# Optimization experiments

Hardware: AMD Instinct MI355X
Metric: run time of the kernel (lower is better)

The kernel has to match this reference:

```python
import jax, jax.numpy as jnp
import numpy as np

N_QUBITS = 4
N_LAYERS = 3
H_IMG = 512

# ---------- 4-qubit statevector simulator, batched over P patches ----------

def _apply_1q(psi, U, w):
    # shared 2x2 gate U on wire w; psi: (P,2,2,2,2)
    psi = jnp.moveaxis(psi, 1 + w, -1)
    psi = jnp.einsum('ij,...j->...i', U, psi)
    return jnp.moveaxis(psi, -1, 1 + w)

def _apply_1q_batched(psi, U, w):
    # per-patch gate U: (P,2,2)
    psi = jnp.moveaxis(psi, 1 + w, -1)
    psi = jnp.einsum('pij,p...j->p...i', U, psi)
    return jnp.moveaxis(psi, -1, 1 + w)

def _apply_cnot(psi, c, t):
    psi = jnp.moveaxis(psi, (1 + c, 1 + t), (-2, -1))
    top = psi[..., 0:1, :]
    bot = psi[..., 1:2, ::-1]  # X on target when control=1
    psi = jnp.concatenate([top, bot], axis=-2)
    return jnp.moveaxis(psi, (-2, -1), (1 + c, 1 + t))

def _rx(theta):
    # AngleEmbedding default rotation='X'; theta: (P,) -> (P,2,2)
    h = theta * 0.5
    c = jnp.cos(h).astype(jnp.complex64)
    s = (-1j * jnp.sin(h)).astype(jnp.complex64)
    return jnp.stack([jnp.stack([c, s], -1), jnp.stack([s, c], -1)], -2)

def _rot(phi, theta, omega):
    # PennyLane Rot = RZ(omega) RY(theta) RZ(phi)
    c = jnp.cos(theta * 0.5)
    s = jnp.sin(theta * 0.5)
    em = jnp.exp(-0.5j * (phi + omega))
    ep = jnp.exp(0.5j * (phi + omega))
    fm = jnp.exp(0.5j * (phi - omega))
    fp = jnp.exp(-0.5j * (phi - omega))
    row0 = jnp.stack([em * c, -fm * s])
    row1 = jnp.stack([fp * s, ep * c])
    return jnp.stack([row0, row1]).astype(jnp.complex64)

def _qsim(inputs, weights):
    # inputs: (P,4) angles; weights: (3,4,3) Rot params -> (P,4) PauliZ expvals
    P = inputs.shape[0]
    psi = jnp.zeros((P, 2, 2, 2, 2), jnp.complex64).at[:, 0, 0, 0, 0].set(1.0)
    for w in range(N_QUBITS):
        psi = _apply_1q_batched(psi, _rx(inputs[:, w]), w)
    for l in range(N_LAYERS):
        for w in range(N_QUBITS):
            psi = _apply_1q(psi, _rot(weights[l, w, 0], weights[l, w, 1], weights[l, w, 2]), w)
        r = (l % (N_QUBITS - 1)) + 1  # StronglyEntanglingLayers default ranges
        for w in range(N_QUBITS):
            psi = _apply_cnot(psi, w, (w + r) % N_QUBITS)
    probs = psi.real ** 2 + psi.imag ** 2  # (P,2,2,2,2)
    ez = []
    for w in range(N_QUBITS):
        axes = tuple(a for a in range(1, 5) if a != 1 + w)
        p = probs.sum(axes)  # (P,2)
        ez.append(p[:, 0] - p[:, 1])
    return jnp.stack(ez, -1)  # (P,4)

def _qconv(x, q_weights):
    img = x[0, 0]  # (H,W)
    a = img[:-1, :-1]; b = img[:-1, 1:]; c = img[1:, :-1]; d = img[1:, 1:]
    Hm, Wm = a.shape
    patches = jnp.stack([a, b, c, d], -1).reshape(-1, 4)  # row-major 2x2 flatten
    ez = _qsim(patches, q_weights)  # (P,4)
    return ez.reshape(Hm, Wm, 4).transpose(2, 0, 1)[None]  # (1,4,Hm,Wm)

# ---------- classical layers ----------

def _conv(x, w, b):
    y = jax.lax.conv_general_dilated(x, w, (1, 1), 'VALID',
                                     dimension_numbers=('NCHW', 'OIHW', 'NCHW'))
    return y + b[None, :, None, None]

def _maxpool2(x):
    return jax.lax.reduce_window(x, -jnp.inf, jax.lax.max,
                                 (1, 1, 2, 2), (1, 1, 2, 2), 'VALID')

def _adaptive_max(x, out):
    H, W = x.shape[-2], x.shape[-1]
    rows = []
    for i in range(out):
        si, ei = (i * H) // out, -(-((i + 1) * H) // out)
        cols = []
        for j in range(out):
            sj, ej = (j * W) // out, -(-((j + 1) * W) // out)
            cols.append(x[..., si:ei, sj:ej].max((-2, -1)))
        rows.append(jnp.stack(cols, -1))
    return jnp.stack(rows, -2)


def setup_inputs() -> dict:
    key = jax.random.key(0)
    ks = jax.random.split(key, 10)
    x = jax.random.normal(ks[0], (1, 1, H_IMG, H_IMG), jnp.float32)
    q_weights = jax.random.uniform(ks[1], (N_LAYERS, N_QUBITS, 3), jnp.float32,
                                   0.0, 2.0 * np.pi)
    conv2_w = jax.random.normal(ks[2], (20, 4, 5, 5), jnp.float32) * 0.05
    conv2_b = jax.random.normal(ks[3], (20,), jnp.float32) * 0.05
    conv3_w = jax.random.normal(ks[4], (40, 20, 3, 3), jnp.float32) * 0.05
    conv3_b = jax.random.normal(ks[5], (40,), jnp.float32) * 0.05
    fc1_w = jax.random.normal(ks[6], (64, 640), jnp.float32) * 0.05
    fc1_b = jax.random.normal(ks[7], (64,), jnp.float32) * 0.05
    fc2_w = jax.random.normal(ks[8], (10, 64), jnp.float32) * 0.05
    fc2_b = jax.random.normal(ks[9], (10,), jnp.float32) * 0.05
    return {'x': x, 'q_weights': q_weights,
            'conv2_w': conv2_w, 'conv2_b': conv2_b,
            'conv3_w': conv3_w, 'conv3_b': conv3_b,
            'fc1_w': fc1_w, 'fc1_b': fc1_b,
            'fc2_w': fc2_w, 'fc2_b': fc2_b}


def reference(x, q_weights, conv2_w, conv2_b, conv3_w, conv3_b,
              fc1_w, fc1_b, fc2_w, fc2_b):
    h = _maxpool2(jax.nn.sigmoid(_qconv(x, q_weights)))        # (1,4,255,255)
    h = _maxpool2(jax.nn.relu(_conv(h, conv2_w, conv2_b)))      # (1,20,125,125)
    h = _adaptive_max(jax.nn.relu(_conv(h, conv3_w, conv3_b)), 4)  # (1,40,4,4)
    h = h.reshape(-1, 640)
    h = jax.nn.relu(h @ fc1_w.T + fc1_b)
    return h @ fc2_w.T + fc2_b  # (1,10)
```

## Files before the change

kernel.cpp:

```cpp
#include <hip/hip_runtime.h>
#include <math.h>

#define IMG 512
#define QO  255
#define QP  256
#define C2H 125
#define C2S 128
#define C3H 123

template<int M_>
__device__ inline void rot_regs(float2* a, float2 U00, float2 U01, float2 U10, float2 U11) {
    #pragma unroll
    for (int s = 0; s < 16; ++s) {
        if (!(s & M_)) {
            float2 a0 = a[s], a1 = a[s | M_];
            a[s]      = make_float2(U00.x*a0.x - U00.y*a0.y + U01.x*a1.x - U01.y*a1.y,
                                    U00.x*a0.y + U00.y*a0.x + U01.x*a1.y + U01.y*a1.x);
            a[s | M_] = make_float2(U10.x*a0.x - U10.y*a0.y + U11.x*a1.x - U11.y*a1.y,
                                    U10.x*a0.y + U10.y*a0.x + U11.x*a1.y + U11.y*a1.x);
        }
    }
}
template<int MC, int MT>
__device__ inline void cnot_regs(float2* a) {
    #pragma unroll
    for (int s = 0; s < 16; ++s) {
        if ((s & MC) && !(s & MT)) {
            float2 t = a[s]; a[s] = a[s | MT]; a[s | MT] = t;
        }
    }
}
__device__ inline void rot_gate_params(float phi, float th, float om,
                                       float2& U00, float2& U01, float2& U10, float2& U11) {
    float ch, sh, ca, sa, cb, sb;
    __sincosf(0.5f * th, &sh, &ch);
    __sincosf(0.5f * (phi + om), &sa, &ca);
    __sincosf(0.5f * (phi - om), &sb, &cb);
    U00 = make_float2( ca*ch, -sa*ch);
    U01 = make_float2(-cb*sh, -sb*sh);
    U10 = make_float2( cb*sh, -sb*sh);
    U11 = make_float2( ca*ch,  sa*ch);
}

__device__ __constant__ int UP1[10] = {0,0,0,0,1,1,1,2,2,3};
__device__ __constant__ int UP2[10] = {0,1,2,3,1,2,3,2,3,3};

__global__ __launch_bounds__(256) void qconv_pool(const float* __restrict__ img,
                                                  const float* __restrict__ qw,
                                                  float* __restrict__ out) {
    __shared__ float2 Ms[256];
    __shared__ float4 G4[100];
    int tid = threadIdx.x;

    if (tid < 16) {
        float2 a[16];
        #pragma unroll
        for (int s = 0; s < 16; ++s) a[s] = make_float2(s == tid ? 1.f : 0.f, 0.f);
        float2 U00, U01, U10, U11;
#define ROTG(L, W) rot_gate_params(qw[((L)*4+(W))*3+0], qw[((L)*4+(W))*3+1], qw[((L)*4+(W))*3+2], U00,U01,U10,U11); \
                   rot_regs<(1 << (3-(W)))>(a, U00, U01, U10, U11);
        ROTG(0,0) ROTG(0,1) ROTG(0,2) ROTG(0,3)
        cnot_regs<8,4>(a); cnot_regs<4,2>(a); cnot_regs<2,1>(a); cnot_regs<1,8>(a);
        ROTG(1,0) ROTG(1,1) ROTG(1,2) ROTG(1,3)
        cnot_regs<8,2>(a); cnot_regs<4,1>(a); cnot_regs<2,8>(a); cnot_regs<1,4>(a);
        ROTG(2,0) ROTG(2,1) ROTG(2,2) ROTG(2,3)
        cnot_regs<8,1>(a); cnot_regs<4,8>(a); cnot_regs<2,4>(a); cnot_regs<1,2>(a);
#undef ROTG
        int pc4 = __popc(tid) & 3;
        #pragma unroll
        for (int row = 0; row < 16; ++row) {
            float2 v = a[row], o;
            if      (pc4 == 0) o = v;
            else if (pc4 == 1) o = make_float2( v.y, -v.x);
            else if (pc4 == 2) o = make_float2(-v.x, -v.y);
            else               o = make_float2(-v.y,  v.x);
            Ms[row * 16 + tid] = o;
        }
    }
    __syncthreads();

    if (tid < 100) {
        int al = tid / 10, be = tid - 10 * (tid / 10);
        int u = UP1[al], up = UP2[al], v = UP1[be], vp = UP2[be];
        float s0 = 0.f, s1 = 0.f, s2 = 0.f, s3 = 0.f;
        for (int ci = 0; ci < 2; ++ci) {
            if (ci == 1 && u == up) break;
            int a1 = ci ? up : u, a2 = ci ? u : up;
            for (int cj = 0; cj < 2; ++cj) {
                if (cj == 1 && v == vp) break;
                int b1 = cj ? vp : v, b2 = cj ? v : vp;
                int k = a1 * 4 + b1, kp = a2 * 4 + b2;
                #pragma unroll
                for (int r = 0; r < 16; ++r) {
                    float2 m1 = Ms[r * 16 + k], m2 = Ms[r * 16 + kp];
                    float p = m1.x * m2.x + m1.y * m2.y;
                    s0 += (r & 8) ? -p : p;
                    s1 += (r & 4) ? -p : p;
                    s2 += (r & 2) ? -p : p;
                    s3 += (r & 1) ? -p : p;
                }
            }
        }
        G4[tid] = make_float4(s0, s1, s2, s3);
    }
    __syncthreads();

    int gid = blockIdx.x * 256 + tid;
    if (gid >= QO * QO) return;
    int i = gid / QO, j = gid - i * QO;
    int r0 = 2 * i, c0 = 2 * j;

    float cs[3][3], sn[3][3];
    #pragma unroll
    for (int rr = 0; rr < 3; ++rr)
        #pragma unroll
        for (int cc = 0; cc < 3; ++cc) {
            float v = img[(r0 + rr) * IMG + c0 + cc];
            __sincosf(0.5f * v, &sn[rr][cc], &cs[rr][cc]);
        }

    float tv[3][2][4];
    #pragma unroll
    for (int rr = 0; rr < 3; ++rr)
        #pragma unroll
        for (int pc = 0; pc < 2; ++pc) {
            tv[rr][pc][0] = cs[rr][pc] * cs[rr][pc+1];
            tv[rr][pc][1] = cs[rr][pc] * sn[rr][pc+1];
            tv[rr][pc][2] = sn[rr][pc] * cs[rr][pc+1];
            tv[rr][pc][3] = sn[rr][pc] * sn[rr][pc+1];
        }

    float mx0 = -1e30f, mx1 = -1e30f, mx2 = -1e30f, mx3 = -1e30f;

    #pragma unroll
    for (int pr = 0; pr < 2; ++pr) {
        #pragma unroll
        for (int pc = 0; pc < 2; ++pc) {
            float q23[10];
            #pragma unroll
            for (int be = 0; be < 10; ++be)
                q23[be] = tv[pr+1][pc][UP1[be]] * tv[pr+1][pc][UP2[be]];

            float e0 = 0.f, e1 = 0.f, e2 = 0.f, e3 = 0.f;
            #pragma unroll
            for (int al = 0; al < 10; ++al) {
                float pa = tv[pr][pc][UP1[al]] * tv[pr][pc][UP2[al]];
                #pragma unroll
                for (int be = 0; be < 10; ++be) {
                    float4 g = G4[al * 10 + be];
                    float pq = pa * q23[be];
                    e0 = fmaf(g.x, pq, e0);
                    e1 = fmaf(g.y, pq, e1);
                    e2 = fmaf(g.z, pq, e2);
                    e3 = fmaf(g.w, pq, e3);
                }
            }
            mx0 = fmaxf(mx0, e0);
            mx1 = fmaxf(mx1, e1);
            mx2 = fmaxf(mx2, e2);
            mx3 = fmaxf(mx3, e3);
        }
    }

    int o = i * QP + j;
    out[0 * QP * QP + o] = 1.f / (1.f + __expf(-mx0));
    out[1 * QP * QP + o] = 1.f / (1.f + __expf(-mx1));
    out[2 * QP * QP + o] = 1.f / (1.f + __expf(-mx2));
    out[3 * QP * QP + o] = 1.f / (1.f + __expf(-mx3));
}

__global__ __launch_bounds__(256) void conv2_pool(const float* __restrict__ in,
                                                  const float* __restrict__ w,
                                                  const float* __restrict__ b,
                                                  float* __restrict__ out,
                                                  float* __restrict__ am) {
    __shared__ float W[100];
    __shared__ float Bv;
    int oc = blockIdx.y;
    if (threadIdx.x < 100) W[threadIdx.x] = w[oc * 100 + threadIdx.x];
    if (threadIdx.x == 0) Bv = b[oc];
    if (blockIdx.x == 0 && oc == 0) {
        for (int e = threadIdx.x; e < 640; e += 256) am[e] = 0.f;
    }
    __syncthreads();

    int sp = blockIdx.x * 256 + threadIdx.x;
    if (sp >= C2H * C2H) return;
    int i = sp / C2H, j = sp - i * C2H;

    float a00 = 0.f, a01 = 0.f, a10 = 0.f, a11 = 0.f;
    #pragma unroll
    for (int ic = 0; ic < 4; ++ic) {
        const float* ip = in + ic * QP * QP + (2 * i) * QP + 2 * j;
        float win[6][6];
        #pragma unroll
        for (int y = 0; y < 6; ++y) {
            #pragma unroll
            for (int h = 0; h < 3; ++h) {
                float2 v = *(const float2*)(ip + y * QP + 2 * h);
                win[y][2*h]   = v.x;
                win[y][2*h+1] = v.y;
            }
        }
        #pragma unroll
        for (int ky = 0; ky < 5; ++ky) {
            #pragma unroll
            for (int kx = 0; kx < 5; ++kx) {
                float wv = W[ic * 25 + ky * 5 + kx];
                a00 = fmaf(win[ky][kx],     wv, a00);
                a01 = fmaf(win[ky][kx+1],   wv, a01);
                a10 = fmaf(win[ky+1][kx],   wv, a10);
                a11 = fmaf(win[ky+1][kx+1], wv, a11);
            }
        }
    }
    float m = fmaxf(fmaxf(a00, a01), fmaxf(a10, a11));
    out[oc * C2H * C2S + i * C2S + j] = fmaxf(m + Bv, 0.f);
}

__global__ __launch_bounds__(256) void conv3_amax(const float* __restrict__ in,
                                                  const float* __restrict__ w,
                                                  const float* __restrict__ b,
                                                  int* __restrict__ am) {
    __shared__ float4 W4[180];
    __shared__ int bm[64];
    int og = blockIdx.y, oc0 = og * 4;
    if (threadIdx.x < 180) {
        int rr = threadIdx.x;
        const float* wb = w + oc0 * 180 + rr;
        W4[rr] = make_float4(wb[0], wb[180], wb[360], wb[540]);
    }
    if (threadIdx.x < 64) bm[threadIdx.x] = 0;
    __syncthreads();

    int sp = blockIdx.x * 256 + threadIdx.x;
    if (sp < C3H * C3H) {
        int y = sp / C3H, x = sp - y * C3H;

        float acc0 = 0.f, acc1 = 0.f, acc2 = 0.f, acc3 = 0.f;
        #pragma unroll
        for (int ic = 0; ic < 20; ++ic) {
            const float* ip = in + ic * C2H * C2S + y * C2S + x;
            float v[3][3];
            #pragma unroll
            for (int ky = 0; ky < 3; ++ky)
                #pragma unroll
                for (int kx = 0; kx < 3; ++kx)
                    v[ky][kx] = ip[ky * C2S + kx];
            #pragma unroll
            for (int kk = 0; kk < 9; ++kk) {
                float4 wv = W4[ic * 9 + kk];
                float iv = v[kk / 3][kk % 3];
                acc0 = fmaf(iv, wv.x, acc0);
                acc1 = fmaf(iv, wv.y, acc1);
                acc2 = fmaf(iv, wv.z, acc2);
                acc3 = fmaf(iv, wv.w, acc3);
            }
        }
        acc0 = fmaxf(acc0 + b[oc0 + 0], 0.f);
        acc1 = fmaxf(acc1 + b[oc0 + 1], 0.f);
        acc2 = fmaxf(acc2 + b[oc0 + 2], 0.f);
        acc3 = fmaxf(acc3 + b[oc0 + 3], 0.f);

        const int bs[4] = {0, 30, 61, 92};
        const int be[4] = {31, 62, 93, 123};
        #pragma unroll
        for (int yb = 0; yb < 4; ++yb) {
            if (y >= bs[yb] && y < be[yb]) {
                #pragma unroll
                for (int xb = 0; xb < 4; ++xb) {
                    if (x >= bs[xb] && x < be[xb]) {
                        int bin = yb * 4 + xb;
                        atomicMax(&bm[0 * 16 + bin], __float_as_int(acc0));
                        atomicMax(&bm[1 * 16 + bin], __float_as_int(acc1));
                        atomicMax(&bm[2 * 16 + bin], __float_as_int(acc2));
                        atomicMax(&bm[3 * 16 + bin], __float_as_int(acc3));
                    }
                }
            }
        }
    }
    __syncthreads();
    if (threadIdx.x < 64) {
        int v = bm[threadIdx.x];
        if (v != 0)
            atomicMax(&am[(oc0 + (threadIdx.x >> 4)) * 16 + (threadIdx.x & 15)], v);
    }
}

__global__ void fc_k(const float* __restrict__ h, const float* __restrict__ w1,
                     const float* __restrict__ b1, const float* __restrict__ w2,
                     const float* __restrict__ b2, float* __restrict__ out) {
    __shared__ float hh[640];
    __shared__ float h1[64];
    int t = threadIdx.x;
    for (int e = t; e < 640; e += 256) hh[e] = h[e];
    __syncthreads();

    int r = t >> 2, q = t & 3;
    const float4* wr = (const float4*)(w1 + r * 640 + q * 160);
    const float*  hp = hh + q * 160;
    float acc = 0.f;
    #pragma unroll 4
    for (int n = 0; n < 40; ++n) {
        float4 wv = wr[n];
        acc = fmaf(wv.x, hp[n*4+0], acc);
        acc = fmaf(wv.y, hp[n*4+1], acc);
        acc = fmaf(wv.z, hp[n*4+2], acc);
        acc = fmaf(wv.w, hp[n*4+3], acc);
    }
    acc += __shfl_xor(acc, 1, 64);
    acc += __shfl_xor(acc, 2, 64);
    if (q == 0) h1[r] = fmaxf(acc + b1[r], 0.f);
    __syncthreads();

    if (t < 10) {
        float o = b2[t];
        #pragma unroll 8
        for (int n = 0; n < 64; ++n) o = fmaf(h1[n], w2[t * 64 + n], o);
        out[t] = o;
    }
}

extern "C" void kernel_launch(void* const* d_in, const int* in_sizes, int n_in,
                              void* d_out, int out_size, void* d_ws, size_t ws_size,
                              hipStream_t stream) {
    const float* x   = (const float*)d_in[0];
    const float* qw  = (const float*)d_in[1];
    const float* c2w = (const float*)d_in[2];
    const float* c2b = (const float*)d_in[3];
    const float* c3w = (const float*)d_in[4];
    const float* c3b = (const float*)d_in[5];
    const float* f1w = (const float*)d_in[6];
    const float* f1b = (const float*)d_in[7];
    const float* f2w = (const float*)d_in[8];
    const float* f2b = (const float*)d_in[9];
    float* out = (float*)d_out;

    float* wsf   = (float*)d_ws;
    float* qout  = wsf;
    float* c2out = qout + 4 * QP * QP;
    float* am    = c2out + 20 * C2H * C2S;

    qconv_pool<<<(QO * QO + 255) / 256, 256, 0, stream>>>(x, qw, qout);
    conv2_pool<<<dim3((C2H * C2H + 255) / 256, 20), 256, 0, stream>>>(qout, c2w, c2b, c2out, am);
    conv3_amax<<<dim3((C3H * C3H + 255) / 256, 10), 256, 0, stream>>>(c2out, c3w, c3b, (int*)am);
    fc_k<<<1, 256, 0, stream>>>(am, f1w, f1b, f2w, f2b, out);
}
```

Baseline: 134.5 us.

## Fuse all four stages into one persistent kernel with grid barriers

Replaces the four kernel launches with a single persistent kernel of 256 blocks. Software grid barriers built on global atomics separate the qconv, conv2, conv3 and FC stages. Shared memory is overlaid through a union, and conv2 and conv3 work is distributed with grid-stride loops. The aim is to remove launch overhead and inter-kernel gaps. In exchange it adds a memset plus barrier spin costs and relies on all 256 blocks being co-resident. qconv needs 255 blocks' worth of work, so one block idles at the barrier, and the fixed 256-block grid limits parallelism in the conv stages.

```diff
diff --git a/kernel.cpp b/kernel.cpp
--- a/kernel.cpp
+++ b/kernel.cpp
@@ -7,6 +7,8 @@
 #define C2H 125
 #define C2S 128
 #define C3H 123
+#define NB  256
+#define NT  256
 
 template<int M_>
 __device__ inline void rot_regs(float2* a, float2 U00, float2 U01, float2 U10, float2 U11) {
@@ -45,11 +47,41 @@
 __device__ __constant__ int UP1[10] = {0,0,0,0,1,1,1,2,2,3};
 __device__ __constant__ int UP2[10] = {0,1,2,3,1,2,3,2,3,3};
 
-__global__ __launch_bounds__(256) void qconv_pool(const float* __restrict__ img,
-                                                  const float* __restrict__ qw,
-                                                  float* __restrict__ out) {
-    __shared__ float2 Ms[256];
-    __shared__ float4 G4[100];
+__device__ __forceinline__ void grid_barrier(int* bar) {
+    __syncthreads();
+    if (threadIdx.x == 0) {
+        __threadfence();
+        if (atomicAdd(bar, 1) == NB - 1) {
+            atomicAdd(bar, NB);
+        } else {
+            while (__hip_atomic_load(bar, __ATOMIC_RELAXED,
+                                     __HIP_MEMORY_SCOPE_AGENT) < 2 * NB)
+                __builtin_amdgcn_s_sleep(8);
+        }
+        __threadfence();
+    }
+    __syncthreads();
+}
+
+union SmemU {
+    struct { float2 Ms[256]; float4 G4[100]; } A;
+    struct { float  W[2000]; float  B[20];  } Bs;
+    struct { float4 W4[180]; int    bm[64]; } C;
+    struct { float  hh[640]; float  h1[64]; } D;
+};
+
+__global__ __launch_bounds__(NT) void fused_net(
+        const float* __restrict__ img, const float* __restrict__ qw,
+        const float* __restrict__ c2w, const float* __restrict__ c2b,
+        const float* __restrict__ c3w, const float* __restrict__ c3b,
+        const float* __restrict__ f1w, const float* __restrict__ f1b,
+        const float* __restrict__ f2w, const float* __restrict__ f2b,
+        float* __restrict__ ws, float* __restrict__ out) {
+    __shared__ SmemU sm;
+    int* bar    = (int*)ws;
+    float* am   = ws + 16;
+    float* qout = ws + 16 + 640;
+    float* c2o  = qout + 4 * QP * QP;
     int tid = threadIdx.x;
 
     if (tid < 16) {
@@ -74,11 +106,10 @@
             else if (pc4 == 1) o = make_float2( v.y, -v.x);
             else if (pc4 == 2) o = make_float2(-v.x, -v.y);
             else               o = make_float2(-v.y,  v.x);
-            Ms[row * 16 + tid] = o;
-        }
-    }
-    __syncthreads();
-
+            sm.A.Ms[row * 16 + tid] = o;
+        }
+    }
+    __syncthreads();
     if (tid < 100) {
         int al = tid / 10, be = tid - 10 * (tid / 10);
         int u = UP1[al], up = UP2[al], v = UP1[be], vp = UP2[be];
@@ -92,7 +123,7 @@
                 int k = a1 * 4 + b1, kp = a2 * 4 + b2;
                 #pragma unroll
                 for (int r = 0; r < 16; ++r) {
-                    float2 m1 = Ms[r * 16 + k], m2 = Ms[r * 16 + kp];
+                    float2 m1 = sm.A.Ms[r * 16 + k], m2 = sm.A.Ms[r * 16 + kp];
                     float p = m1.x * m2.x + m1.y * m2.y;
                     s0 += (r & 8) ? -p : p;
                     s1 += (r & 4) ? -p : p;
@@ -101,224 +132,197 @@
                 }
             }
         }
-        G4[tid] = make_float4(s0, s1, s2, s3);
-    }
-    __syncthreads();
-
-    int gid = blockIdx.x * 256 + tid;
-    if (gid >= QO * QO) return;
-    int i = gid / QO, j = gid - i * QO;
-    int r0 = 2 * i, c0 = 2 * j;
-
-    float cs[3][3], sn[3][3];
-    #pragma unroll
-    for (int rr = 0; rr < 3; ++rr)
+        sm.A.G4[tid] = make_float4(s0, s1, s2, s3);
+    }
+    __syncthreads();
+
+    {
+        int gid = blockIdx.x * NT + tid;
+        if (gid < QO * QO) {
+            int i = gid / QO, j = gid - i * QO;
+            int r0 = 2 * i, c0 = 2 * j;
+            float cs[3][3], sn[3][3];
+            #pragma unroll
+            for (int rr = 0; rr < 3; ++rr)
+                #pragma unroll
+                for (int cc = 0; cc < 3; ++cc) {
+                    float v = img[(r0 + rr) * IMG + c0 + cc];
+                    __sincosf(0.5f * v, &sn[rr][cc], &cs[rr][cc]);
+                }
+            float tv[3][2][4];
+            #pragma unroll
+            for (int rr = 0; rr < 3; ++rr)
+                #pragma unroll
+                for (int pc = 0; pc < 2; ++pc) {
+                    tv[rr][pc][0] = cs[rr][pc] * cs[rr][pc+1];
+                    tv[rr][pc][1] = cs[rr][pc] * sn[rr][pc+1];
+                    tv[rr][pc][2] = sn[rr][pc] * cs[rr][pc+1];
+                    tv[rr][pc][3] = sn[rr][pc] * sn[rr][pc+1];
+                }
+            float mx0 = -1e30f, mx1 = -1e30f, mx2 = -1e30f, mx3 = -1e30f;
+            #pragma unroll
+            for (int pr = 0; pr < 2; ++pr) {
+                #pragma unroll
+                for (int pc = 0; pc < 2; ++pc) {
+                    float q23[10];
+                    #pragma unroll
+                    for (int be = 0; be < 10; ++be)
+                        q23[be] = tv[pr+1][pc][UP1[be]] * tv[pr+1][pc][UP2[be]];
+                    float e0 = 0.f, e1 = 0.f, e2 = 0.f, e3 = 0.f;
+                    #pragma unroll
+                    for (int al = 0; al < 10; ++al) {
+                        float pa = tv[pr][pc][UP1[al]] * tv[pr][pc][UP2[al]];
+                        #pragma unroll
+                        for (int be = 0; be < 10; ++be) {
+                            float4 g = sm.A.G4[al * 10 + be];
+                            float pq = pa * q23[be];
+                            e0 = fmaf(g.x, pq, e0);
+                            e1 = fmaf(g.y, pq, e1);
+                            e2 = fmaf(g.z, pq, e2);
+                            e3 = fmaf(g.w, pq, e3);
+                        }
+                    }
+                    mx0 = fmaxf(mx0, e0); mx1 = fmaxf(mx1, e1);
+                    mx2 = fmaxf(mx2, e2); mx3 = fmaxf(mx3, e3);
+                }
+            }
+            int o = i * QP + j;
+            qout[0 * QP * QP + o] = 1.f / (1.f + __expf(-mx0));
+            qout[1 * QP * QP + o] = 1.f / (1.f + __expf(-mx1));
+            qout[2 * QP * QP + o] = 1.f / (1.f + __expf(-mx2));
+            qout[3 * QP * QP + o] = 1.f / (1.f + __expf(-mx3));
+        }
+    }
+    grid_barrier(bar + 0);
+
+    for (int e = tid; e < 2000; e += NT) sm.Bs.W[e] = c2w[e];
+    if (tid < 20) sm.Bs.B[tid] = c2b[tid];
+    __syncthreads();
+    for (int e = blockIdx.x * NT + tid; e < 20 * C2H * C2H; e += NB * NT) {
+        int oc = e / (C2H * C2H);
+        int sp = e - oc * (C2H * C2H);
+        int i = sp / C2H, j = sp - i * C2H;
+        float a00 = 0.f, a01 = 0.f, a10 = 0.f, a11 = 0.f;
         #pragma unroll
-        for (int cc = 0; cc < 3; ++cc) {
-            float v = img[(r0 + rr) * IMG + c0 + cc];
-            __sincosf(0.5f * v, &sn[rr][cc], &cs[rr][cc]);
-        }
-
-    float tv[3][2][4];
-    #pragma unroll
-    for (int rr = 0; rr < 3; ++rr)
-        #pragma unroll
-        for (int pc = 0; pc < 2; ++pc) {
-            tv[rr][pc][0] = cs[rr][pc] * cs[rr][pc+1];
-            tv[rr][pc][1] = cs[rr][pc] * sn[rr][pc+1];
-            tv[rr][pc][2] = sn[rr][pc] * cs[rr][pc+1];
-            tv[rr][pc][3] = sn[rr][pc] * sn[rr][pc+1];
-        }
-
-    float mx0 = -1e30f, mx1 = -1e30f, mx2 = -1e30f, mx3 = -1e30f;
-
-    #pragma unroll
-    for (int pr = 0; pr < 2; ++pr) {
-        #pragma unroll
-        for (int pc = 0; pc < 2; ++pc) {
-            float q23[10];
-            #pragma unroll
-            for (int be = 0; be < 10; ++be)
-                q23[be] = tv[pr+1][pc][UP1[be]] * tv[pr+1][pc][UP2[be]];
-
-            float e0 = 0.f, e1 = 0.f, e2 = 0.f, e3 = 0.f;
-            #pragma unroll
-            for (int al = 0; al < 10; ++al) {
-                float pa = tv[pr][pc][UP1[al]] * tv[pr][pc][UP2[al]];
-                #pragma unroll
-                for (int be = 0; be < 10; ++be) {
-                    float4 g = G4[al * 10 + be];
-                    float pq = pa * q23[be];
-                    e0 = fmaf(g.x, pq, e0);
-                    e1 = fmaf(g.y, pq, e1);
-                    e2 = fmaf(g.z, pq, e2);
-                    e3 = fmaf(g.w, pq, e3);
-                }
-            }
-            mx0 = fmaxf(mx0, e0);
-            mx1 = fmaxf(mx1, e1);
-            mx2 = fmaxf(mx2, e2);
-            mx3 = fmaxf(mx3, e3);
-        }
-    }
-
-    int o = i * QP + j;
-    out[0 * QP * QP + o] = 1.f / (1.f + __expf(-mx0));
-    out[1 * QP * QP + o] = 1.f / (1.f + __expf(-mx1));
-    out[2 * QP * QP + o] = 1.f / (1.f + __expf(-mx2));
-    out[3 * QP * QP + o] = 1.f / (1.f + __expf(-mx3));
-}
-
-__global__ __launch_bounds__(256) void conv2_pool(const float* __restrict__ in,
-                                                  const float* __restrict__ w,
-                                                  const float* __restrict__ b,
-                                                  float* __restrict__ out,
-                                                  float* __restrict__ am) {
-    __shared__ float W[100];
-    __shared__ float Bv;
-    int oc = blockIdx.y;
-    if (threadIdx.x < 100) W[threadIdx.x] = w[oc * 100 + threadIdx.x];
-    if (threadIdx.x == 0) Bv = b[oc];
-    if (blockIdx.x == 0 && oc == 0) {
-        for (int e = threadIdx.x; e < 640; e += 256) am[e] = 0.f;
-    }
-    __syncthreads();
-
-    int sp = blockIdx.x * 256 + threadIdx.x;
-    if (sp >= C2H * C2H) return;
-    int i = sp / C2H, j = sp - i * C2H;
-
-    float a00 = 0.f, a01 = 0.f, a10 = 0.f, a11 = 0.f;
-    #pragma unroll
-    for (int ic = 0; ic < 4; ++ic) {
-        const float* ip = in + ic * QP * QP + (2 * i) * QP + 2 * j;
-        float win[6][6];
-        #pragma unroll
-        for (int y = 0; y < 6; ++y) {
-            #pragma unroll
-            for (int h = 0; h < 3; ++h) {
-                float2 v = *(const float2*)(ip + y * QP + 2 * h);
-                win[y][2*h]   = v.x;
-                win[y][2*h+1] = v.y;
-            }
-        }
-        #pragma unroll
-        for (int ky = 0; ky < 5; ++ky) {
-            #pragma unroll
-            for (int kx = 0; kx < 5; ++kx) {
-                float wv = W[ic * 25 + ky * 5 + kx];
-                a00 = fmaf(win[ky][kx],     wv, a00);
-                a01 = fmaf(win[ky][kx+1],   wv, a01);
-                a10 = fmaf(win[ky+1][kx],   wv, a10);
-                a11 = fmaf(win[ky+1][kx+1], wv, a11);
-            }
-        }
-    }
-    float m = fmaxf(fmaxf(a00, a01), fmaxf(a10, a11));
-    out[oc * C2H * C2S + i * C2S + j] = fmaxf(m + Bv, 0.f);
-}
-
-__global__ __launch_bounds__(256) void conv3_amax(const float* __restrict__ in,
-                                                  const float* __restrict__ w,
-                                                  const float* __restrict__ b,
-                                                  int* __restrict__ am) {
-    __shared__ float4 W4[180];
-    __shared__ int bm[64];
-    int og = blockIdx.y, oc0 = og * 4;
-    if (threadIdx.x < 180) {
-        int rr = threadIdx.x;
-        const float* wb = w + oc0 * 180 + rr;
-        W4[rr] = make_float4(wb[0], wb[180], wb[360], wb[540]);
-    }
-    if (threadIdx.x < 64) bm[threadIdx.x] = 0;
-    __syncthreads();
-
-    int sp = blockIdx.x * 256 + threadIdx.x;
-    if (sp < C3H * C3H) {
-        int y = sp / C3H, x = sp - y * C3H;
-
-        float acc0 = 0.f, acc1 = 0.f, acc2 = 0.f, acc3 = 0.f;
-        #pragma unroll
-        for (int ic = 0; ic < 20; ++ic) {
-            const float* ip = in + ic * C2H * C2S + y * C2S + x;
-            float v[3][3];
-            #pragma unroll
-            for (int ky = 0; ky < 3; ++ky)
-                #pragma unroll
-                for (int kx = 0; kx < 3; ++kx)
-                    v[ky][kx] = ip[ky * C2S + kx];
-            #pragma unroll
-            for (int kk = 0; kk < 9; ++kk) {
-                float4 wv = W4[ic * 9 + kk];
-                float iv = v[kk / 3][kk % 3];
-                acc0 = fmaf(iv, wv.x, acc0);
-                acc1 = fmaf(iv, wv.y, acc1);
-                acc2 = fmaf(iv, wv.z, acc2);
-                acc3 = fmaf(iv, wv.w, acc3);
-            }
-        }
-        acc0 = fmaxf(acc0 + b[oc0 + 0], 0.f);
-        acc1 = fmaxf(acc1 + b[oc0 + 1], 0.f);
-        acc2 = fmaxf(acc2 + b[oc0 + 2], 0.f);
-        acc3 = fmaxf(acc3 + b[oc0 + 3], 0.f);
-
-        const int bs[4] = {0, 30, 61, 92};
-        const int be[4] = {31, 62, 93, 123};
-        #pragma unroll
-        for (int yb = 0; yb < 4; ++yb) {
-            if (y >= bs[yb] && y < be[yb]) {
-                #pragma unroll
-                for (int xb = 0; xb < 4; ++xb) {
-                    if (x >= bs[xb] && x < be[xb]) {
-                        int bin = yb * 4 + xb;
-                        atomicMax(&bm[0 * 16 + bin], __float_as_int(acc0));
-                        atomicMax(&bm[1 * 16 + bin], __float_as_int(acc1));
-                        atomicMax(&bm[2 * 16 + bin], __float_as_int(acc2));
-                        atomicMax(&bm[3 * 16 + bin], __float_as_int(acc3));
+        for (int ic = 0; ic < 4; ++ic) {
+            const float* ip = qout + ic * QP * QP + (2 * i) * QP + 2 * j;
+            float win[6][6];
+            #pragma unroll
+            for (int y = 0; y < 6; ++y) {
+                #pragma unroll
+                for (int h = 0; h < 3; ++h) {
+                    float2 v = *(const float2*)(ip + y * QP + 2 * h);
+                    win[y][2*h]   = v.x;
+                    win[y][2*h+1] = v.y;
+                }
+            }
+            const float* wp = &sm.Bs.W[(oc * 4 + ic) * 25];
+            #pragma unroll
+            for (int ky = 0; ky < 5; ++ky) {
+                #pragma unroll
+                for (int kx = 0; kx < 5; ++kx) {
+                    float wv = wp[ky * 5 + kx];
+                    a00 = fmaf(win[ky][kx],     wv, a00);
+                    a01 = fmaf(win[ky][kx+1],   wv, a01);
+                    a10 = fmaf(win[ky+1][kx],   wv, a10);
+                    a11 = fmaf(win[ky+1][kx+1], wv, a11);
+                }
+            }
+        }
+        float m = fmaxf(fmaxf(a00, a01), fmaxf(a10, a11));
+        c2o[oc * C2H * C2S + i * C2S + j] = fmaxf(m + sm.Bs.B[oc], 0.f);
+    }
+    grid_barrier(bar + 1);
+
+    for (int chunk = blockIdx.x; chunk < 600; chunk += NB) {
+        int og = chunk / 60, sb = chunk - og * 60, oc0 = og * 4;
+        __syncthreads();
+        if (tid < 180) {
+            const float* wb = c3w + oc0 * 180 + tid;
+            sm.C.W4[tid] = make_float4(wb[0], wb[180], wb[360], wb[540]);
+        }
+        if (tid < 64) sm.C.bm[tid] = 0;
+        __syncthreads();
+        int sp = sb * NT + tid;
+        if (sp < C3H * C3H) {
+            int y = sp / C3H, x = sp - y * C3H;
+            float acc0 = 0.f, acc1 = 0.f, acc2 = 0.f, acc3 = 0.f;
+            #pragma unroll
+            for (int ic = 0; ic < 20; ++ic) {
+                const float* ip = c2o + ic * C2H * C2S + y * C2S + x;
+                float v[3][3];
+                #pragma unroll
+                for (int ky = 0; ky < 3; ++ky)
+                    #pragma unroll
+                    for (int kx = 0; kx < 3; ++kx)
+                        v[ky][kx] = ip[ky * C2S + kx];
+                #pragma unroll
+                for (int kk = 0; kk < 9; ++kk) {
+                    float4 wv = sm.C.W4[ic * 9 + kk];
+                    float iv = v[kk / 3][kk % 3];
+                    acc0 = fmaf(iv, wv.x, acc0);
+                    acc1 = fmaf(iv, wv.y, acc1);
+                    acc2 = fmaf(iv, wv.z, acc2);
+                    acc3 = fmaf(iv, wv.w, acc3);
+                }
+            }
+            acc0 = fmaxf(acc0 + c3b[oc0 + 0], 0.f);
+            acc1 = fmaxf(acc1 + c3b[oc0 + 1], 0.f);
+            acc2 = fmaxf(acc2 + c3b[oc0 + 2], 0.f);
+            acc3 = fmaxf(acc3 + c3b[oc0 + 3], 0.f);
+            const int bs[4] = {0, 30, 61, 92};
+            const int be[4] = {31, 62, 93, 123};
+            #pragma unroll
+            for (int yb = 0; yb < 4; ++yb) {
+                if (y >= bs[yb] && y < be[yb]) {
+                    #pragma unroll
+                    for (int xb = 0; xb < 4; ++xb) {
+                        if (x >= bs[xb] && x < be[xb]) {
+                            int bin = yb * 4 + xb;
+                            atomicMax(&sm.C.bm[0 * 16 + bin], __float_as_int(acc0));
+                            atomicMax(&sm.C.bm[1 * 16 + bin], __float_as_int(acc1));
+                            atomicMax(&sm.C.bm[2 * 16 + bin], __float_as_int(acc2));
+                            atomicMax(&sm.C.bm[3 * 16 + bin], __float_as_int(acc3));
+                        }
                     }
                 }
             }
         }
-    }
-    __syncthreads();
-    if (threadIdx.x < 64) {
-        int v = bm[threadIdx.x];
-        if (v != 0)
-            atomicMax(&am[(oc0 + (threadIdx.x >> 4)) * 16 + (threadIdx.x & 15)], v);
-    }
-}
-
-__global__ void fc_k(const float* __restrict__ h, const float* __restrict__ w1,
-                     const float* __restrict__ b1, const float* __restrict__ w2,
-                     const float* __restrict__ b2, float* __restrict__ out) {
-    __shared__ float hh[640];
-    __shared__ float h1[64];
-    int t = threadIdx.x;
-    for (int e = t; e < 640; e += 256) hh[e] = h[e];
-    __syncthreads();
-
-    int r = t >> 2, q = t & 3;
-    const float4* wr = (const float4*)(w1 + r * 640 + q * 160);
-    const float*  hp = hh + q * 160;
-    float acc = 0.f;
-    #pragma unroll 4
-    for (int n = 0; n < 40; ++n) {
-        float4 wv = wr[n];
-        acc = fmaf(wv.x, hp[n*4+0], acc);
-        acc = fmaf(wv.y, hp[n*4+1], acc);
-        acc = fmaf(wv.z, hp[n*4+2], acc);
-        acc = fmaf(wv.w, hp[n*4+3], acc);
-    }
-    acc += __shfl_xor(acc, 1, 64);
-    acc += __shfl_xor(acc, 2, 64);
-    if (q == 0) h1[r] = fmaxf(acc + b1[r], 0.f);
-    __syncthreads();
-
-    if (t < 10) {
-        float o = b2[t];
+        __syncthreads();
+        if (tid < 64) {
+            int v = sm.C.bm[tid];
+            if (v != 0)
+                atomicMax((int*)&am[(oc0 + (tid >> 4)) * 16 + (tid & 15)], v);
+        }
+    }
+    grid_barrier(bar + 2);
+
+    if (blockIdx.x != 0) return;
+    for (int e = tid; e < 640; e += NT) sm.D.hh[e] = am[e];
+    __syncthreads();
+    {
+        int r = tid >> 2, q = tid & 3;
+        const float4* wr = (const float4*)(f1w + r * 640 + q * 160);
+        const float*  hp = sm.D.hh + q * 160;
+        float acc = 0.f;
+        #pragma unroll 4
+        for (int n = 0; n < 40; ++n) {
+            float4 wv = wr[n];
+            acc = fmaf(wv.x, hp[n*4+0], acc);
+            acc = fmaf(wv.y, hp[n*4+1], acc);
+            acc = fmaf(wv.z, hp[n*4+2], acc);
+            acc = fmaf(wv.w, hp[n*4+3], acc);
+        }
+        acc += __shfl_xor(acc, 1, 64);
+        acc += __shfl_xor(acc, 2, 64);
+        if (q == 0) sm.D.h1[r] = fmaxf(acc + f1b[r], 0.f);
+    }
+    __syncthreads();
+    if (tid < 10) {
+        float o = f2b[tid];
         #pragma unroll 8
-        for (int n = 0; n < 64; ++n) o = fmaf(h1[n], w2[t * 64 + n], o);
-        out[t] = o;
+        for (int n = 0; n < 64; ++n) o = fmaf(sm.D.h1[n], f2w[tid * 64 + n], o);
+        out[tid] = o;
     }
 }
 
@@ -335,15 +339,9 @@
     const float* f1b = (const float*)d_in[7];
     const float* f2w = (const float*)d_in[8];
     const float* f2b = (const float*)d_in[9];
-    float* out = (float*)d_out;
-
-    float* wsf   = (float*)d_ws;
-    float* qout  = wsf;
-    float* c2out = qout + 4 * QP * QP;
-    float* am    = c2out + 20 * C2H * C2S;
-
-    qconv_pool<<<(QO * QO + 255) / 256, 256, 0, stream>>>(x, qw, qout);
-    conv2_pool<<<dim3((C2H * C2H + 255) / 256, 20), 256, 0, stream>>>(qout, c2w, c2b, c2out, am);
-    conv3_amax<<<dim3((C3H * C3H + 255) / 256, 10), 256, 0, stream>>>(c2out, c3w, c3b, (int*)am);
-    fc_k<<<1, 256, 0, stream>>>(am, f1w, f1b, f2w, f2b, out);
-}
+
+    hipMemsetAsync(d_ws, 0, (16 + 640) * sizeof(float), stream);
+    fused_net<<<NB, NT, 0, stream>>>(x, qw, c2w, c2b, c3w, c3b,
+                                     f1w, f1b, f2w, f2b,
+                                     (float*)d_ws, (float*)d_out);
+}
```

Measured after the change: 220.6 us. 1.64x slower.

## Hoist quantum gram matrix into its own kernel and split pool window across lanes

Applied to the files above, without the earlier changes.

The per-block statevector simulation and Gram-matrix construction move into a single-block build_G kernel whose result is written to workspace and loaded by every qconv block. The quantum-conv kernel now gives each of the four 2x2 pool positions its own thread and combines their results with wavefront shuffles for the max. This removes redundant per-block gate simulation, which every block used to repeat, and spreads the 400-FMA inner loop over four times as many threads for more parallelism. The cost is an extra kernel launch, some redundant sin/cos on shared pixels, and four times as many threads.

```diff
diff --git a/kernel.cpp b/kernel.cpp
--- a/kernel.cpp
+++ b/kernel.cpp
@@ -45,13 +45,9 @@
 __device__ __constant__ int UP1[10] = {0,0,0,0,1,1,1,2,2,3};
 __device__ __constant__ int UP2[10] = {0,1,2,3,1,2,3,2,3,3};
 
-__global__ __launch_bounds__(256) void qconv_pool(const float* __restrict__ img,
-                                                  const float* __restrict__ qw,
-                                                  float* __restrict__ out) {
+__global__ void build_G(const float* __restrict__ qw, float4* __restrict__ gG) {
     __shared__ float2 Ms[256];
-    __shared__ float4 G4[100];
     int tid = threadIdx.x;
-
     if (tid < 16) {
         float2 a[16];
         #pragma unroll
@@ -78,7 +74,6 @@
         }
     }
     __syncthreads();
-
     if (tid < 100) {
         int al = tid / 10, be = tid - 10 * (tid / 10);
         int u = UP1[al], up = UP2[al], v = UP1[be], vp = UP2[be];
@@ -101,72 +96,67 @@
                 }
             }
         }
-        G4[tid] = make_float4(s0, s1, s2, s3);
-    }
+        gG[tid] = make_float4(s0, s1, s2, s3);
+    }
+}
+
+__global__ __launch_bounds__(256) void qconv_pool(const float* __restrict__ img,
+                                                  const float4* __restrict__ gG,
+                                                  float* __restrict__ out) {
+    __shared__ float4 G4[100];
+    int tid = threadIdx.x;
+    if (tid < 100) G4[tid] = gG[tid];
     __syncthreads();
 
     int gid = blockIdx.x * 256 + tid;
-    if (gid >= QO * QO) return;
-    int i = gid / QO, j = gid - i * QO;
-    int r0 = 2 * i, c0 = 2 * j;
-
-    float cs[3][3], sn[3][3];
-    #pragma unroll
-    for (int rr = 0; rr < 3; ++rr)
-        #pragma unroll
-        for (int cc = 0; cc < 3; ++cc) {
-            float v = img[(r0 + rr) * IMG + c0 + cc];
-            __sincosf(0.5f * v, &sn[rr][cc], &cs[rr][cc]);
-        }
-
-    float tv[3][2][4];
-    #pragma unroll
-    for (int rr = 0; rr < 3; ++rr)
-        #pragma unroll
-        for (int pc = 0; pc < 2; ++pc) {
-            tv[rr][pc][0] = cs[rr][pc] * cs[rr][pc+1];
-            tv[rr][pc][1] = cs[rr][pc] * sn[rr][pc+1];
-            tv[rr][pc][2] = sn[rr][pc] * cs[rr][pc+1];
-            tv[rr][pc][3] = sn[rr][pc] * sn[rr][pc+1];
-        }
-
-    float mx0 = -1e30f, mx1 = -1e30f, mx2 = -1e30f, mx3 = -1e30f;
-
-    #pragma unroll
-    for (int pr = 0; pr < 2; ++pr) {
-        #pragma unroll
-        for (int pc = 0; pc < 2; ++pc) {
-            float q23[10];
-            #pragma unroll
-            for (int be = 0; be < 10; ++be)
-                q23[be] = tv[pr+1][pc][UP1[be]] * tv[pr+1][pc][UP2[be]];
-
-            float e0 = 0.f, e1 = 0.f, e2 = 0.f, e3 = 0.f;
-            #pragma unroll
-            for (int al = 0; al < 10; ++al) {
-                float pa = tv[pr][pc][UP1[al]] * tv[pr][pc][UP2[al]];
-                #pragma unroll
-                for (int be = 0; be < 10; ++be) {
-                    float4 g = G4[al * 10 + be];
-                    float pq = pa * q23[be];
-                    e0 = fmaf(g.x, pq, e0);
-                    e1 = fmaf(g.y, pq, e1);
-                    e2 = fmaf(g.z, pq, e2);
-                    e3 = fmaf(g.w, pq, e3);
-                }
-            }
-            mx0 = fmaxf(mx0, e0);
-            mx1 = fmaxf(mx1, e1);
-            mx2 = fmaxf(mx2, e2);
-            mx3 = fmaxf(mx3, e3);
-        }
-    }
-
-    int o = i * QP + j;
-    out[0 * QP * QP + o] = 1.f / (1.f + __expf(-mx0));
-    out[1 * QP * QP + o] = 1.f / (1.f + __expf(-mx1));
-    out[2 * QP * QP + o] = 1.f / (1.f + __expf(-mx2));
-    out[3 * QP * QP + o] = 1.f / (1.f + __expf(-mx3));
+    int pixel = gid >> 2, p = gid & 3;
+    if (pixel >= QO * QO) return;
+    int i = pixel / QO, j = pixel - i * QO;
+    int pr = p >> 1, pc = p & 1;
+    const float* ip = img + (2 * i + pr) * IMG + (2 * j + pc);
+
+    float x00 = ip[0], x01 = ip[1], x10 = ip[IMG], x11 = ip[IMG + 1];
+    float s0, c0, s1, c1, s2, c2, s3, c3;
+    __sincosf(0.5f * x00, &s0, &c0);
+    __sincosf(0.5f * x01, &s1, &c1);
+    __sincosf(0.5f * x10, &s2, &c2);
+    __sincosf(0.5f * x11, &s3, &c3);
+
+    float t01[4] = {c0 * c1, c0 * s1, s0 * c1, s0 * s1};
+    float t23[4] = {c2 * c3, c2 * s3, s2 * c3, s2 * s3};
+    float q01[10], q23[10];
+    #pragma unroll
+    for (int al = 0; al < 10; ++al) q01[al] = t01[UP1[al]] * t01[UP2[al]];
+    #pragma unroll
+    for (int be = 0; be < 10; ++be) q23[be] = t23[UP1[be]] * t23[UP2[be]];
+
+    float e0 = 0.f, e1 = 0.f, e2 = 0.f, e3 = 0.f;
+    #pragma unroll
+    for (int al = 0; al < 10; ++al) {
+        float pa = q01[al];
+        #pragma unroll
+        for (int be = 0; be < 10; ++be) {
+            float4 g = G4[al * 10 + be];
+            float pq = pa * q23[be];
+            e0 = fmaf(g.x, pq, e0);
+            e1 = fmaf(g.y, pq, e1);
+            e2 = fmaf(g.z, pq, e2);
+            e3 = fmaf(g.w, pq, e3);
+        }
+    }
+
+    e0 = fmaxf(e0, __shfl_xor(e0, 1, 64)); e0 = fmaxf(e0, __shfl_xor(e0, 2, 64));
+    e1 = fmaxf(e1, __shfl_xor(e1, 1, 64)); e1 = fmaxf(e1, __shfl_xor(e1, 2, 64));
+    e2 = fmaxf(e2, __shfl_xor(e2, 1, 64)); e2 = fmaxf(e2, __shfl_xor(e2, 2, 64));
+    e3 = fmaxf(e3, __shfl_xor(e3, 1, 64)); e3 = fmaxf(e3, __shfl_xor(e3, 2, 64));
+
+    if (p == 0) {
+        int o = i * QP + j;
+        out[0 * QP * QP + o] = 1.f / (1.f + __expf(-e0));
+        out[1 * QP * QP + o] = 1.f / (1.f + __expf(-e1));
+        out[2 * QP * QP + o] = 1.f / (1.f + __expf(-e2));
+        out[3 * QP * QP + o] = 1.f / (1.f + __expf(-e3));
+    }
 }
 
 __global__ __launch_bounds__(256) void conv2_pool(const float* __restrict__ in,
@@ -226,9 +216,8 @@
     __shared__ int bm[64];
     int og = blockIdx.y, oc0 = og * 4;
     if (threadIdx.x < 180) {
-        int rr = threadIdx.x;
-        const float* wb = w + oc0 * 180 + rr;
-        W4[rr] = make_float4(wb[0], wb[180], wb[360], wb[540]);
+        const float* wb = w + oc0 * 180 + threadIdx.x;
+        W4[threadIdx.x] = make_float4(wb[0], wb[180], wb[360], wb[540]);
     }
     if (threadIdx.x < 64) bm[threadIdx.x] = 0;
     __syncthreads();
@@ -338,11 +327,13 @@
     float* out = (float*)d_out;
 
     float* wsf   = (float*)d_ws;
-    float* qout  = wsf;
+    float4* gG   = (float4*)d_ws;
+    float* am    = wsf + 400;
+    float* qout  = am + 640;
     float* c2out = qout + 4 * QP * QP;
-    float* am    = c2out + 20 * C2H * C2S;
-
-    qconv_pool<<<(QO * QO + 255) / 256, 256, 0, stream>>>(x, qw, qout);
+
+    build_G<<<1, 128, 0, stream>>>(qw, gG);
+    qconv_pool<<<(4 * QO * QO + 255) / 256, 256, 0, stream>>>(x, gG, qout);
     conv2_pool<<<dim3((C2H * C2H + 255) / 256, 20), 256, 0, stream>>>(qout, c2w, c2b, c2out, am);
     conv3_amax<<<dim3((C3H * C3H + 255) / 256, 10), 256, 0, stream>>>(c2out, c3w, c3b, (int*)am);
     fc_k<<<1, 256, 0, stream>>>(am, f1w, f1b, f2w, f2b, out);
```

Measured after the change: 139.9 us. 4.0% more time.
